# Optimization experiments

Hardware: AMD Instinct MI355X
Metric: run time of the kernel (lower is better)

The kernel has to match this reference:

```python
import jax, jax.numpy as jnp
import numpy as np

B = 2097152  # batch
H = 9        # hidden width
N_MID = 19   # fc2..fc20


def setup_inputs() -> dict:
    key = jax.random.key(0)
    ks = jax.random.split(key, 8)
    x = jax.random.normal(ks[0], (B, 2), dtype=jnp.float32)
    # PyTorch Linear init: U(-1/sqrt(fan_in), 1/sqrt(fan_in))
    def lin(k, out_f, in_f):
        kw, kb = jax.random.split(k)
        bound = 1.0 / np.sqrt(in_f)
        W = jax.random.uniform(kw, (out_f, in_f), jnp.float32, -bound, bound)
        b = jax.random.uniform(kb, (out_f,), jnp.float32, -bound, bound)
        return W, b
    W1, b1 = lin(ks[1], H, 2)
    # stacked middle layers fc2..fc20: [19, 9, 9] / [19, 9]
    kmids = jax.random.split(ks[2], N_MID)
    Wmid = jnp.stack([lin(k, H, H)[0] for k in kmids])
    bmid = jnp.stack([lin(jax.random.fold_in(k, 1), H, H)[1] for k in kmids])
    W21, b21 = lin(ks[3], 2, H)
    return {"x": x, "W1": W1, "b1": b1, "Wmid": Wmid, "bmid": bmid,
            "W21": W21, "b21": b21}


def reference(x, W1, b1, Wmid, bmid, W21, b21):
    h = jax.nn.elu(x @ W1.T + b1)  # [B, 9]
    def layer(h, wb):
        W, b = wb
        return jax.nn.elu(h @ W.T + b), None
    h, _ = jax.lax.scan(layer, h, (Wmid, bmid))
    logits = h @ W21.T + b21  # [B, 2]
    return jax.nn.log_softmax(logits, axis=1)
```

## Files before the change

### kernel.cpp

```cpp
#include <hip/hip_runtime.h>


typedef _Float16 half4 __attribute__((ext_vector_type(4)));
typedef _Float16 h2 __attribute__((ext_vector_type(2)));
typedef __fp16 fp16x2 __attribute__((ext_vector_type(2)));
typedef float float4v __attribute__((ext_vector_type(4)));
typedef unsigned int uint2v __attribute__((ext_vector_type(2)));

extern "C" __device__ _Float16 __ocml_exp2_f16(_Float16);

constexpr int H   = 9;
constexpr int NL  = 21;
constexpr int TPW = 8;
constexpr int BLK = 256;

__global__ void build_frags(const float* __restrict__ W1, const float* __restrict__ b1,
                            const float* __restrict__ Wmid, const float* __restrict__ bmid,
                            const float* __restrict__ W21, const float* __restrict__ b21,
                            _Float16* __restrict__ ws) {
    const float LOG2E = 1.4426950408889634f;
    const float LN2   = 0.6931471805599453f;
    int l = blockIdx.x;
    int p = threadIdx.x;
    int m = p & 15;
    int g = p >> 4;
    for (int j = 0; j < 4; ++j) {
        int k = g * 4 + j;
        float v = 0.0f;
        if (l == 0) {
            if (m < H && k < 2)       v = LOG2E * W1[m * 2 + k];
            else if (m < H && k == 9) v = LOG2E * b1[m];
        } else if (l <= 19) {
            int li = l - 1;
            if (m < H && k < H)       v = Wmid[li * 81 + m * 9 + k];
            else if (m < H && k == 9) v = LOG2E * bmid[li * 9 + m];
        } else {
            if (m < 2 && k < H)       v = LN2 * W21[m * 9 + k];
            else if (m < 2 && k == 9) v = b21[m];
        }
        ws[l * 256 + p * 4 + j] = (_Float16)v;
    }
}

__device__ __forceinline__ half4 act_to_b(float4v d, unsigned bias_or) {
    const h2 Z  = {(_Float16)0.f, (_Float16)0.f};
    const h2 L  = {(_Float16)1.4426950408889634f, (_Float16)1.4426950408889634f};
    const h2 nL = {(_Float16)-1.4426950408889634f, (_Float16)-1.4426950408889634f};
    h2 p0 = __builtin_bit_cast(h2, __builtin_amdgcn_cvt_pkrtz(d[0], d[1]));
    h2 p1 = __builtin_bit_cast(h2, __builtin_amdgcn_cvt_pkrtz(d[2], d[3]));
    h2 t0 = __builtin_elementwise_min(p0, Z);
    h2 t1 = __builtin_elementwise_min(p1, Z);
    h2 e0, e1;
    e0[0] = __ocml_exp2_f16(t0[0]);
    e0[1] = __ocml_exp2_f16(t0[1]);
    e1[0] = __ocml_exp2_f16(t1[0]);
    e1[1] = __ocml_exp2_f16(t1[1]);
    h2 g0 = __builtin_elementwise_max(p0, __builtin_elementwise_fma(e0, L, nL));
    h2 g1 = __builtin_elementwise_max(p1, __builtin_elementwise_fma(e1, L, nL));
    uint2v u;
    u[0] = __builtin_bit_cast(unsigned, g0) | bias_or;
    u[1] = __builtin_bit_cast(unsigned, g1);
    return __builtin_bit_cast(half4, u);
}

__device__ __forceinline__ half4 x_to_b(float2 xv, unsigned g0_sel, unsigned bias_or) {
    unsigned ux = __builtin_bit_cast(unsigned, __builtin_amdgcn_cvt_pkrtz(xv.x, xv.y));
    uint2v u;
    u[0] = (ux & g0_sel) | bias_or;
    u[1] = 0u;
    return __builtin_bit_cast(half4, u);
}

__device__ __forceinline__ void write_out(float4v d, float* __restrict__ out,
                                          long long row, int lane) {
    if (lane < 16) {
        float l0 = d[0], l1 = d[1];
        float m  = fmaxf(l0, l1);
        float e0 = __expf(l0 - m);
        float e1 = __expf(l1 - m);
        float lse = m + __logf(e0 + e1);
        ((float2*)out)[row] = make_float2(l0 - lse, l1 - lse);
    }
}

__global__ __launch_bounds__(BLK) void mlp_mfma(const float* __restrict__ x,
                                                const _Float16* __restrict__ ws,
                                                float* __restrict__ out) {
    const int lane = threadIdx.x & 63;
    const int wave = (blockIdx.x * BLK + threadIdx.x) >> 6;
    const int col  = lane & 15;
    const int grp  = lane >> 4;

    half4 A[NL];
    const half4* wsv = (const half4*)ws;
    #pragma unroll
    for (int l = 0; l < NL; ++l) A[l] = wsv[l * 64 + lane];

    const unsigned bias_or = (grp == 2) ? 0x3C000000u : 0u;
    const unsigned g0_sel  = (grp == 0) ? 0xFFFFFFFFu : 0u;

    #pragma unroll 1
    for (int t = 0; t < TPW; t += 2) {
        const long long rowa = ((long long)wave * TPW + t) * 16 + col;
        const long long rowb = rowa + 16;

        float2 xa = ((const float2*)x)[rowa];
        float2 xb = ((const float2*)x)[rowb];
        half4 ba = x_to_b(xa, g0_sel, bias_or);
        half4 bb = x_to_b(xb, g0_sel, bias_or);

        float4v da, db;
        #pragma unroll
        for (int l = 0; l < NL; ++l) {
            da = __builtin_amdgcn_mfma_f32_16x16x16f16(A[l], ba, (float4v){0.f,0.f,0.f,0.f}, 0, 0, 0);
            db = __builtin_amdgcn_mfma_f32_16x16x16f16(A[l], bb, (float4v){0.f,0.f,0.f,0.f}, 0, 0, 0);
            if (l < NL - 1) {
                ba = act_to_b(da, bias_or);
                bb = act_to_b(db, bias_or);
            }
        }
        write_out(da, out, rowa, lane);
        write_out(db, out, rowb, lane);
    }
}

extern "C" void kernel_launch(void* const* d_in, const int* in_sizes, int n_in,
                              void* d_out, int out_size, void* d_ws, size_t ws_size,
                              hipStream_t stream) {
    const float* x    = (const float*)d_in[0];
    const float* W1   = (const float*)d_in[1];
    const float* b1   = (const float*)d_in[2];
    const float* Wmid = (const float*)d_in[3];
    const float* bmid = (const float*)d_in[4];
    const float* W21  = (const float*)d_in[5];
    const float* b21  = (const float*)d_in[6];
    float* out = (float*)d_out;
    _Float16* ws = (_Float16*)d_ws;

    build_frags<<<NL, 64, 0, stream>>>(W1, b1, Wmid, bmid, W21, b21, ws);

    const int nrows = in_sizes[0] / 2;
    const int tiles = nrows / 16;
    const int waves = tiles / TPW;
    const int blocks = waves * 64 / BLK;
    mlp_mfma<<<blocks, BLK, 0, stream>>>(x, ws, out);
}
```

Measured before the change: 190.5 us.

## Split ELU into relu and exp terms folded into K=32 MFMA weights

Rewrites ELU as max(x,0) + exp(min(x,0)) - 1 and moves the constant -1 and log2e scaling into the next layer's weights and bias, so the activation only computes relu and exp2. The positive and exponential parts are fed as separate K slots of a wider 16x16x32 f16 MFMA, and the output layout skips every fourth accumulator row so each lane evaluates three exponentials instead of four. This cuts VALU work in the activation in exchange for an MFMA with twice the K depth and twice the register footprint for the weight fragments.

Result: faster. 179.1 us (-6.0%).

```diff
diff --git a/kernel.cpp b/kernel.cpp
--- a/kernel.cpp
+++ b/kernel.cpp
@@ -1,11 +1,10 @@
 #include <hip/hip_runtime.h>
 
 
-typedef _Float16 half4 __attribute__((ext_vector_type(4)));
+typedef _Float16 half8 __attribute__((ext_vector_type(8)));
 typedef _Float16 h2 __attribute__((ext_vector_type(2)));
-typedef __fp16 fp16x2 __attribute__((ext_vector_type(2)));
 typedef float float4v __attribute__((ext_vector_type(4)));
-typedef unsigned int uint2v __attribute__((ext_vector_type(2)));
+typedef unsigned int uint4v __attribute__((ext_vector_type(4)));
 
 extern "C" __device__ _Float16 __ocml_exp2_f16(_Float16);
 
@@ -18,57 +17,86 @@
                             const float* __restrict__ Wmid, const float* __restrict__ bmid,
                             const float* __restrict__ W21, const float* __restrict__ b21,
                             _Float16* __restrict__ ws) {
-    const float LOG2E = 1.4426950408889634f;
-    const float LN2   = 0.6931471805599453f;
-    int l = blockIdx.x;
-    int p = threadIdx.x;
-    int m = p & 15;
-    int g = p >> 4;
-    for (int j = 0; j < 4; ++j) {
-        int k = g * 4 + j;
+    const float L   = 1.4426950408889634f;
+    const float LN2 = 0.6931471805599453f;
+    int l    = blockIdx.x;
+    int lane = threadIdx.x;
+    int row  = lane & 15;
+    int g    = lane >> 4;
+    bool orow = ((row & 3) != 3) && (row < 12);
+    int  o    = row - (row >> 2);
+    for (int j = 0; j < 8; ++j) {
+        int k = g * 8 + j;
         float v = 0.0f;
         if (l == 0) {
-            if (m < H && k < 2)       v = LOG2E * W1[m * 2 + k];
-            else if (m < H && k == 9) v = LOG2E * b1[m];
+            if (orow && k < 2)        v = L * W1[o * 2 + k];
+            else if (orow && k == 24) v = L * b1[o];
         } else if (l <= 19) {
-            int li = l - 1;
-            if (m < H && k < H)       v = Wmid[li * 81 + m * 9 + k];
-            else if (m < H && k == 9) v = LOG2E * bmid[li * 9 + m];
+            const float* W = Wmid + (l - 1) * 81;
+            const float* b = bmid + (l - 1) * 9;
+            if (orow) {
+                if (j < 3 && g < 3) {
+                    int r_in = g * 4 + j;
+                    int i = r_in - (r_in >> 2);
+                    v = W[o * 9 + i];
+                } else if (j >= 4 && j < 7 && g < 3) {
+                    int r_in = g * 4 + (j - 4);
+                    int i = r_in - (r_in >> 2);
+                    v = L * W[o * 9 + i];
+                } else if (k == 24) {
+                    float s = 0.0f;
+                    for (int i = 0; i < H; ++i) s += W[o * 9 + i];
+                    v = L * (b[o] - s);
+                }
+            }
         } else {
-            if (m < 2 && k < H)       v = LN2 * W21[m * 9 + k];
-            else if (m < 2 && k == 9) v = b21[m];
+            if (row < 2) {
+                if (j < 3 && g < 3) {
+                    int r_in = g * 4 + j;
+                    int i = r_in - (r_in >> 2);
+                    v = LN2 * W21[row * 9 + i];
+                } else if (j >= 4 && j < 7 && g < 3) {
+                    int r_in = g * 4 + (j - 4);
+                    int i = r_in - (r_in >> 2);
+                    v = W21[row * 9 + i];
+                } else if (k == 24) {
+                    float s = 0.0f;
+                    for (int i = 0; i < H; ++i) s += W21[row * 9 + i];
+                    v = b21[row] - s;
+                }
+            }
         }
-        ws[l * 256 + p * 4 + j] = (_Float16)v;
+        ws[l * 512 + lane * 8 + j] = (_Float16)v;
     }
 }
 
-__device__ __forceinline__ half4 act_to_b(float4v d, unsigned bias_or) {
-    const h2 Z  = {(_Float16)0.f, (_Float16)0.f};
-    const h2 L  = {(_Float16)1.4426950408889634f, (_Float16)1.4426950408889634f};
-    const h2 nL = {(_Float16)-1.4426950408889634f, (_Float16)-1.4426950408889634f};
-    h2 p0 = __builtin_bit_cast(h2, __builtin_amdgcn_cvt_pkrtz(d[0], d[1]));
-    h2 p1 = __builtin_bit_cast(h2, __builtin_amdgcn_cvt_pkrtz(d[2], d[3]));
-    h2 t0 = __builtin_elementwise_min(p0, Z);
-    h2 t1 = __builtin_elementwise_min(p1, Z);
-    h2 e0, e1;
-    e0[0] = __ocml_exp2_f16(t0[0]);
-    e0[1] = __ocml_exp2_f16(t0[1]);
-    e1[0] = __ocml_exp2_f16(t1[0]);
-    e1[1] = __ocml_exp2_f16(t1[1]);
-    h2 g0 = __builtin_elementwise_max(p0, __builtin_elementwise_fma(e0, L, nL));
-    h2 g1 = __builtin_elementwise_max(p1, __builtin_elementwise_fma(e1, L, nL));
-    uint2v u;
-    u[0] = __builtin_bit_cast(unsigned, g0) | bias_or;
-    u[1] = __builtin_bit_cast(unsigned, g1);
-    return __builtin_bit_cast(half4, u);
+__device__ __forceinline__ half8 act_to_b(float4v d, unsigned bias_or) {
+    const h2 Z = {(_Float16)0.f, (_Float16)0.f};
+    h2 p01 = __builtin_bit_cast(h2, __builtin_amdgcn_cvt_pkrtz(d[0], d[1]));
+    h2 p2x = __builtin_bit_cast(h2, __builtin_amdgcn_cvt_pkrtz(d[2], d[3]));
+    h2 r01 = __builtin_elementwise_max(p01, Z);
+    h2 r2x = __builtin_elementwise_max(p2x, Z);
+    h2 t01 = __builtin_elementwise_min(p01, Z);
+    h2 t2x = __builtin_elementwise_min(p2x, Z);
+    h2 e01;
+    e01[0] = __ocml_exp2_f16(t01[0]);
+    e01[1] = __ocml_exp2_f16(t01[1]);
+    h2 e2x = t2x;
+    e2x[0] = __ocml_exp2_f16(t2x[0]);
+    uint4v u;
+    u[0] = __builtin_bit_cast(unsigned, r01) | bias_or;
+    u[1] = __builtin_bit_cast(unsigned, r2x);
+    u[2] = __builtin_bit_cast(unsigned, e01);
+    u[3] = __builtin_bit_cast(unsigned, e2x);
+    return __builtin_bit_cast(half8, u);
 }
 
-__device__ __forceinline__ half4 x_to_b(float2 xv, unsigned g0_sel, unsigned bias_or) {
+__device__ __forceinline__ half8 x_to_b(float2 xv, unsigned g0_sel, unsigned bias_or) {
     unsigned ux = __builtin_bit_cast(unsigned, __builtin_amdgcn_cvt_pkrtz(xv.x, xv.y));
-    uint2v u;
+    uint4v u;
     u[0] = (ux & g0_sel) | bias_or;
-    u[1] = 0u;
-    return __builtin_bit_cast(half4, u);
+    u[1] = 0u; u[2] = 0u; u[3] = 0u;
+    return __builtin_bit_cast(half8, u);
 }
 
 __device__ __forceinline__ void write_out(float4v d, float* __restrict__ out,
@@ -88,15 +116,15 @@
                                                 float* __restrict__ out) {
     const int lane = threadIdx.x & 63;
     const int wave = (blockIdx.x * BLK + threadIdx.x) >> 6;
+    const int grp  = lane >> 4;
     const int col  = lane & 15;
-    const int grp  = lane >> 4;
 
-    half4 A[NL];
-    const half4* wsv = (const half4*)ws;
+    half8 A[NL];
+    const half8* wsv = (const half8*)ws;
     #pragma unroll
     for (int l = 0; l < NL; ++l) A[l] = wsv[l * 64 + lane];
 
-    const unsigned bias_or = (grp == 2) ? 0x3C000000u : 0u;
+    const unsigned bias_or = (grp == 3) ? 0x00003C00u : 0u;
     const unsigned g0_sel  = (grp == 0) ? 0xFFFFFFFFu : 0u;
 
     #pragma unroll 1
@@ -106,14 +134,14 @@
 
         float2 xa = ((const float2*)x)[rowa];
         float2 xb = ((const float2*)x)[rowb];
-        half4 ba = x_to_b(xa, g0_sel, bias_or);
-        half4 bb = x_to_b(xb, g0_sel, bias_or);
+        half8 ba = x_to_b(xa, g0_sel, bias_or);
+        half8 bb = x_to_b(xb, g0_sel, bias_or);
 
         float4v da, db;
         #pragma unroll
         for (int l = 0; l < NL; ++l) {
-            da = __builtin_amdgcn_mfma_f32_16x16x16f16(A[l], ba, (float4v){0.f,0.f,0.f,0.f}, 0, 0, 0);
-            db = __builtin_amdgcn_mfma_f32_16x16x16f16(A[l], bb, (float4v){0.f,0.f,0.f,0.f}, 0, 0, 0);
+            da = __builtin_amdgcn_mfma_f32_16x16x32_f16(A[l], ba, (float4v){0.f,0.f,0.f,0.f}, 0, 0, 0);
+            db = __builtin_amdgcn_mfma_f32_16x16x32_f16(A[l], bb, (float4v){0.f,0.f,0.f,0.f}, 0, 0, 0);
             if (l < NL - 1) {
                 ba = act_to_b(da, bias_or);
                 bb = act_to_b(db, bias_or);
```
